# Optimization experiments

Hardware: AMD Instinct MI355X
Metric: run time of the kernel (lower is better)

Reference implementation:

```python
import jax, jax.numpy as jnp
import numpy as np

B, S, IN = 4, 4096, 2048
E, D, A, R = 16, 128, 128, 4  # num_experts, expert_vector_dim, attn_dim, mlp_rank
LN_EPS = 1e-5


def _ln2(x, g, b):
    # LayerNorm over the last two dims [E, D] jointly (torch nn.LayerNorm([E, D]))
    mu = x.mean(axis=(-2, -1), keepdims=True)
    var = ((x - mu) ** 2).mean(axis=(-2, -1), keepdims=True)
    return (x - mu) * jax.lax.rsqrt(var + LN_EPS) * g + b


def setup_inputs() -> dict:
    key = jax.random.key(0)
    ks = jax.random.split(key, 8)
    f32 = jnp.float32
    return {
        "hidden_states": jax.random.normal(ks[0], (B, S, IN), f32),
        "expert_embedding": jax.random.normal(ks[1], (E, D), f32) * 0.02,
        "ln_gamma": jnp.ones((E, D), f32),
        "ln_beta": jnp.zeros((E, D), f32),
        "Wv_w": jax.random.normal(ks[2], (E, IN), f32) * 0.02,
        "Wv_b": jnp.zeros((E,), f32),
        "mlp_w1": jax.random.normal(ks[3], (R, IN), f32) * 0.02,
        "mlp_b1": jnp.zeros((R,), f32),
        "mlp_w2": jax.random.normal(ks[4], (E * D, R), f32) * 0.02,
        "mlp_b2": jnp.zeros((E * D,), f32),
        "te_Wq": jax.random.normal(ks[5], (A, D), f32) * 0.05,
        "te_Wk": jax.random.normal(ks[6], (A, D), f32) * 0.05,
        "top_k": 2,
    }


def reference(hidden_states, expert_embedding, ln_gamma, ln_beta, Wv_w, Wv_b,
              mlp_w1, mlp_b1, mlp_w2, mlp_b2, te_Wq, te_Wk, top_k):
    # global expert vectors, layernormed over [E, D]: (E, D)
    ge = _ln2(expert_embedding[None, None], ln_gamma, ln_beta)[0, 0]
    # input gate = W_v(hidden): (B, S, E)
    input_gate = jnp.einsum('bsi,ei->bse', hidden_states, Wv_w) + Wv_b
    # TE mlp -> dynamic per-token expert vectors: (B, S, E, D)
    h = jax.nn.relu(jnp.einsum('bsi,ri->bsr', hidden_states, mlp_w1) + mlp_b1)
    dyn = (jnp.einsum('bsr,or->bso', h, mlp_w2) + mlp_b2).reshape(B, S, E, D)
    dyn = _ln2(dyn, ln_gamma, ln_beta)
    # attention-style routing: Q from dyn experts, K from global experts
    q = jnp.einsum('bsed,ad->bsea', dyn, te_Wq)     # (B, S, E, A)
    k = jnp.einsum('ed,ad->ea', ge, te_Wk)          # (E, A)
    scale = 1.0 / float(np.sqrt(A))
    sim = jax.nn.softmax(jnp.einsum('bsqa,ka->bsqk', q, k) * scale, axis=-1)
    gate = jnp.einsum('bsqk,bsk->bsq', sim, input_gate)
    rw = jax.nn.softmax(gate, axis=-1)              # (B, S, E)
    # top-k masking + sharpened softmax (temperature 0.1)
    vals, idx = jax.lax.top_k(rw, top_k)            # (B, S, k)
    oh = jax.nn.one_hot(idx, E, dtype=rw.dtype)     # (B, S, k, E)
    scattered = jnp.einsum('bske,bsk->bse', oh, vals)
    keep = oh.sum(axis=-2) > 0
    neg = jnp.finfo(rw.dtype).min
    masked = jnp.where(keep, scattered, neg)
    return jax.nn.softmax(masked / 0.1, axis=-1)
```

## Files before the change

kernel.cpp:

```cpp
#include <hip/hip_runtime.h>
#include <math.h>

#define NTOK   16384
#define INDIM  2048
#define NEXP   16
#define DDIM   128
#define NROWS  20

#define WS_PKT  0
#define WS_D1K  1024
#define WS_GQK  1280
#define WS_BQK  1536
#define WS_SCAL 1792
#define WS_TOT  1818

#define SIM_SCALE 0.08838834764831845f

__global__ __launch_bounds__(256) void hr_pre2(
    const float* __restrict__ ee, const float* __restrict__ gam,
    const float* __restrict__ bta, const float* __restrict__ w2,
    const float* __restrict__ b2, const float* __restrict__ wq,
    const float* __restrict__ wk, float* __restrict__ ws)
{
    const int tid  = threadIdx.x;
    const int bx   = blockIdx.x;
    const int lane = tid & 63;
    const int wave = tid >> 6;

    if (bx == 16) {
        __shared__ float sacc[26];
        if (tid < 26) sacc[tid] = 0.f;
        __syncthreads();
        float pa[26];
        #pragma unroll
        for (int j = 0; j < 26; ++j) pa[j] = 0.f;
        for (int i = tid; i < 2048; i += 256) {
            float b = b2[i];
            float4 w4 = *(const float4*)(w2 + i * 4);
            float wr[4] = {w4.x, w4.y, w4.z, w4.w};
            pa[0] += b;
            pa[1] += b * b;
            #pragma unroll
            for (int r = 0; r < 4; ++r) {
                pa[2 + r] += wr[r];
                pa[6 + r] += b * wr[r];
                #pragma unroll
                for (int r2 = 0; r2 < 4; ++r2) pa[10 + r * 4 + r2] += wr[r] * wr[r2];
            }
        }
        #pragma unroll
        for (int j = 0; j < 26; ++j) {
            float v = pa[j];
            v += __shfl_xor(v, 32);
            v += __shfl_xor(v, 16);
            v += __shfl_xor(v, 8);
            v += __shfl_xor(v, 4);
            v += __shfl_xor(v, 2);
            v += __shfl_xor(v, 1);
            if (lane == 0) atomicAdd(&sacc[j], v);
        }
        __syncthreads();
        if (tid < 26) ws[WS_SCAL + tid] = sacc[tid] * (1.f / 2048.f);
        return;
    }

    const int e2 = bx;
    __shared__ float sge[128];
    __shared__ float sK[128];
    __shared__ float sWqK[128];
    __shared__ float sred[8];

    float v8[8];
    float s = 0.f;
    #pragma unroll
    for (int j = 0; j < 8; ++j) {
        v8[j] = ee[tid + j * 256];
        s += v8[j];
    }
    s += __shfl_xor(s, 32); s += __shfl_xor(s, 16); s += __shfl_xor(s, 8);
    s += __shfl_xor(s, 4);  s += __shfl_xor(s, 2);  s += __shfl_xor(s, 1);
    if (lane == 0) sred[wave] = s;
    __syncthreads();
    const float mu = (sred[0] + sred[1] + sred[2] + sred[3]) * (1.f / 2048.f);
    float q = 0.f;
    #pragma unroll
    for (int j = 0; j < 8; ++j) {
        float d = v8[j] - mu;
        q += d * d;
    }
    q += __shfl_xor(q, 32); q += __shfl_xor(q, 16); q += __shfl_xor(q, 8);
    q += __shfl_xor(q, 4);  q += __shfl_xor(q, 2);  q += __shfl_xor(q, 1);
    if (lane == 0) sred[4 + wave] = q;
    __syncthreads();
    const float rsq = rsqrtf((sred[4] + sred[5] + sred[6] + sred[7]) * (1.f / 2048.f) + 1e-5f);

    if (tid < 128) {
        int idx = (e2 << 7) + tid;
        sge[tid] = (ee[idx] - mu) * rsq * gam[idx] + bta[idx];
    }
    __syncthreads();

    {
        int a = tid >> 1, half = tid & 1;
        const float* wr = wk + (a << 7) + (half << 6);
        const float* gg = sge + (half << 6);
        float acc = 0.f;
        #pragma unroll 8
        for (int j = 0; j < 64; ++j) acc = fmaf(gg[j], wr[j], acc);
        acc += __shfl_xor(acc, 1);
        if (half == 0) sK[a] = acc;
    }
    __syncthreads();

    {
        int d = tid >> 1, half = tid & 1;
        float acc = 0.f;
        #pragma unroll 8
        for (int j = 0; j < 64; ++j) {
            int a = (half << 6) + j;
            acc = fmaf(wq[(a << 7) + d], sK[a], acc);
        }
        acc += __shfl_xor(acc, 1);
        if (half == 0) sWqK[d] = acc;
    }
    __syncthreads();

    {
        int o = tid >> 2, qd = tid & 3;
        int r = o >> 4, e = o & 15;
        float acc = 0.f;
        #pragma unroll 8
        for (int j = 0; j < 32; ++j) {
            int d  = (qd << 5) + j;
            int ed = (e << 7) + d;
            acc = fmaf(w2[ed * 4 + r] * gam[ed], sWqK[d], acc);
        }
        acc += __shfl_xor(acc, 1);
        acc += __shfl_xor(acc, 2);
        if (qd == 0) ws[WS_PKT + (e2 << 6) + (r << 4) + e] = acc;
    }

    if (tid < 192) {
        int kind = tid >> 6;
        int e    = (tid >> 2) & 15;
        int qd   = tid & 3;
        float acc = 0.f;
        #pragma unroll 8
        for (int j = 0; j < 32; ++j) {
            int d  = (qd << 5) + j;
            int ed = (e << 7) + d;
            float w = sWqK[d];
            float t = (kind == 0) ? b2[ed] * gam[ed]
                    : (kind == 1) ? gam[ed]
                                  : bta[ed];
            acc = fmaf(t, w, acc);
        }
        acc += __shfl_xor(acc, 1);
        acc += __shfl_xor(acc, 2);
        if (qd == 0) ws[WS_D1K + (kind << 8) + (e2 << 4) + e] = acc;
    }
}

__global__ __launch_bounds__(256) void hr_main(
    const float* __restrict__ hidden, const float* __restrict__ wv,
    const float* __restrict__ wvb, const float* __restrict__ w1,
    const float* __restrict__ b1, const float* __restrict__ tab,
    float* __restrict__ out)
{
    __shared__ float tabs[1824];
    __shared__ float red[16][20];
    const int tid  = threadIdx.x;
    const int wave = tid >> 6;
    const int lane = tid & 63;

    for (int i = tid; i < WS_TOT; i += 256) tabs[i] = tab[i];

    const int tok0 = (blockIdx.x << 4) + (wave << 2);
    const float* hb = hidden + (size_t)tok0 * INDIM + (lane << 2);

    float acc[NROWS][4];
    #pragma unroll
    for (int w = 0; w < NROWS; ++w) {
        acc[w][0] = 0.f; acc[w][1] = 0.f; acc[w][2] = 0.f; acc[w][3] = 0.f;
    }

    for (int c = 0; c < 8; ++c) {
        const int off = c << 8;
        float4 h0 = *(const float4*)(hb + off);
        float4 h1 = *(const float4*)(hb + off + INDIM);
        float4 h2 = *(const float4*)(hb + off + 2 * INDIM);
        float4 h3 = *(const float4*)(hb + off + 3 * INDIM);
        #pragma unroll
        for (int w = 0; w < NROWS; ++w) {
            const float* wr = (w < 16) ? (wv + (w << 11)) : (w1 + ((w - 16) << 11));
            float4 wf = *(const float4*)(wr + off + (lane << 2));
            acc[w][0] = fmaf(h0.x, wf.x, fmaf(h0.y, wf.y, fmaf(h0.z, wf.z, fmaf(h0.w, wf.w, acc[w][0]))));
            acc[w][1] = fmaf(h1.x, wf.x, fmaf(h1.y, wf.y, fmaf(h1.z, wf.z, fmaf(h1.w, wf.w, acc[w][1]))));
            acc[w][2] = fmaf(h2.x, wf.x, fmaf(h2.y, wf.y, fmaf(h2.z, wf.z, fmaf(h2.w, wf.w, acc[w][2]))));
            acc[w][3] = fmaf(h3.x, wf.x, fmaf(h3.y, wf.y, fmaf(h3.z, wf.z, fmaf(h3.w, wf.w, acc[w][3]))));
        }
    }

    #pragma unroll
    for (int w = 0; w < NROWS; ++w) {
        #pragma unroll
        for (int t = 0; t < 4; ++t) {
            float v = acc[w][t];
            v += __shfl_xor(v, 32);
            v += __shfl_xor(v, 16);
            v += __shfl_xor(v, 8);
            v += __shfl_xor(v, 4);
            v += __shfl_xor(v, 2);
            v += __shfl_xor(v, 1);
            acc[w][t] = v;
        }
    }
    if (lane < 4) {
        const int row = (wave << 2) + lane;
        #pragma unroll
        for (int w = 0; w < NROWS; ++w) {
            float v = (lane == 0) ? acc[w][0]
                    : (lane == 1) ? acc[w][1]
                    : (lane == 2) ? acc[w][2] : acc[w][3];
            red[row][w] = v;
        }
    }
    __syncthreads();

    const int tok = tid >> 4;
    const int e   = tid & 15;

    float ig[16];
    #pragma unroll
    for (int j = 0; j < 16; ++j) ig[j] = red[tok][j] + wvb[j];
    float h[4];
    #pragma unroll
    for (int r = 0; r < 4; ++r) h[r] = fmaxf(red[tok][16 + r] + b1[r], 0.f);

    float muT = tabs[WS_SCAL + 0];
    float e2m = tabs[WS_SCAL + 1];
    #pragma unroll
    for (int r = 0; r < 4; ++r) {
        muT = fmaf(h[r], tabs[WS_SCAL + 2 + r], muT);
        e2m = fmaf(2.f * h[r], tabs[WS_SCAL + 6 + r], e2m);
        #pragma unroll
        for (int r2 = 0; r2 < 4; ++r2)
            e2m = fmaf(h[r] * h[r2], tabs[WS_SCAL + 10 + r * 4 + r2], e2m);
    }
    const float var = e2m - muT * muT;
    const float rsq = rsqrtf(var + 1e-5f);

    float sv[16];
    #pragma unroll
    for (int e2 = 0; e2 < 16; ++e2) {
        float s = tabs[WS_D1K + (e2 << 4) + e];
        s = fmaf(h[0], tabs[(e2 << 6) + e], s);
        s = fmaf(h[1], tabs[(e2 << 6) + 16 + e], s);
        s = fmaf(h[2], tabs[(e2 << 6) + 32 + e], s);
        s = fmaf(h[3], tabs[(e2 << 6) + 48 + e], s);
        s = fmaf(-muT, tabs[WS_GQK + (e2 << 4) + e], s);
        sv[e2] = (rsq * s + tabs[WS_BQK + (e2 << 4) + e]) * SIM_SCALE;
    }
    float mx = sv[0];
    #pragma unroll
    for (int e2 = 1; e2 < 16; ++e2) mx = fmaxf(mx, sv[e2]);
    float den = 0.f, gate = 0.f;
    #pragma unroll
    for (int e2 = 0; e2 < 16; ++e2) {
        float p = __expf(sv[e2] - mx);
        den += p;
        gate = fmaf(p, ig[e2], gate);
    }
    gate /= den;

    float gm = gate;
    gm = fmaxf(gm, __shfl_xor(gm, 1));
    gm = fmaxf(gm, __shfl_xor(gm, 2));
    gm = fmaxf(gm, __shfl_xor(gm, 4));
    gm = fmaxf(gm, __shfl_xor(gm, 8));
    float ex = __expf(gate - gm);
    float es = ex;
    es += __shfl_xor(es, 1);
    es += __shfl_xor(es, 2);
    es += __shfl_xor(es, 4);
    es += __shfl_xor(es, 8);
    const float rw = ex / es;

    float v1 = rw; int i1 = e;
    #pragma unroll
    for (int m = 1; m <= 8; m <<= 1) {
        float ov = __shfl_xor(v1, m);
        int   oi = __shfl_xor(i1, m);
        if (ov > v1 || (ov == v1 && oi < i1)) { v1 = ov; i1 = oi; }
    }
    float v2 = (e == i1) ? -INFINITY : rw; int i2 = e;
    #pragma unroll
    for (int m = 1; m <= 8; m <<= 1) {
        float ov = __shfl_xor(v2, m);
        int   oi = __shfl_xor(i2, m);
        if (ov > v2 || (ov == v2 && oi < i2)) { v2 = ov; i2 = oi; }
    }

    float oval = 0.f;
    if (e == i1 || e == i2) {
        float t = __expf((v2 - v1) * 10.f);
        oval = (e == i1) ? (1.f / (1.f + t)) : (t / (1.f + t));
    }
    out[(((size_t)blockIdx.x << 4) + tok) * 16 + e] = oval;
}

extern "C" void kernel_launch(void* const* d_in, const int* in_sizes, int n_in,
                              void* d_out, int out_size, void* d_ws, size_t ws_size,
                              hipStream_t stream)
{
    const float* hidden = (const float*)d_in[0];
    const float* ee     = (const float*)d_in[1];
    const float* gam    = (const float*)d_in[2];
    const float* bta    = (const float*)d_in[3];
    const float* wv     = (const float*)d_in[4];
    const float* wvb    = (const float*)d_in[5];
    const float* w1     = (const float*)d_in[6];
    const float* b1     = (const float*)d_in[7];
    const float* w2     = (const float*)d_in[8];
    const float* b2     = (const float*)d_in[9];
    const float* wq     = (const float*)d_in[10];
    const float* wk     = (const float*)d_in[11];
    float* out = (float*)d_out;
    float* ws  = (float*)d_ws;

    hipLaunchKernelGGL(hr_pre2, dim3(17), dim3(256), 0, stream,
                       ee, gam, bta, w2, b2, wq, wk, ws);
    hipLaunchKernelGGL(hr_main, dim3(NTOK / 16), dim3(256), 0, stream,
                       hidden, wv, wvb, w1, b1, ws, out);
}
```

Measured before the change: 267.7 us.

## Double-buffer weight rows into LDS via async global_load_lds and restructure reduction

The main GEMV loop now stages the 20 weight rows per 256-column chunk into LDS with asynchronous global-to-LDS loads, double-buffered so the next chunk's weights and hidden values load while the current chunk computes. The cross-lane reduction is cut to two shuffles, with the rest finished through a padded LDS transpose and summed per (token,row). The routing table is read straight from global memory instead of being copied into shared memory. Launch bounds request 3 blocks per CU. This trades redundant per-wave global weight loads and long shuffle chains for more LDS traffic and extra barriers.

```diff
diff --git a/kernel.cpp b/kernel.cpp
--- a/kernel.cpp
+++ b/kernel.cpp
@@ -3,9 +3,9 @@
 
 #define NTOK   16384
 #define INDIM  2048
-#define NEXP   16
-#define DDIM   128
 #define NROWS  20
+#define CHUNK  256
+#define NCH    8
 
 #define WS_PKT  0
 #define WS_D1K  1024
@@ -15,6 +15,53 @@
 #define WS_TOT  1818
 
 #define SIM_SCALE 0.08838834764831845f
+
+#define LBUF1   5120
+#define LRED2_STRIDE 324
+#define LRED    5440
+
+__device__ __forceinline__ void async16(const float* g, float* l) {
+    __builtin_amdgcn_global_load_lds(
+        (const __attribute__((address_space(1))) void*)g,
+        (__attribute__((address_space(3))) void*)l, 16, 0, 0);
+}
+
+__device__ __forceinline__ void stage_rows(const float* __restrict__ wv,
+                                           const float* __restrict__ w1,
+                                           float* ldsbase, int wave, int lane,
+                                           int goff) {
+    const int l4 = lane << 2;
+    #pragma unroll
+    for (int j = 0; j < 5; ++j) {
+        const int r = wave + (j << 2);
+        const float* src = (j < 4) ? (wv + (r << 11)) : (w1 + ((r - 16) << 11));
+        async16(src + goff + l4, ldsbase + r * CHUNK + l4);
+    }
+}
+
+__device__ __forceinline__ void load_h(float4* hr, const float* hb, int c) {
+    const float* p = hb + (c << 8);
+    hr[0] = *(const float4*)(p);
+    hr[1] = *(const float4*)(p + INDIM);
+    hr[2] = *(const float4*)(p + 2 * INDIM);
+    hr[3] = *(const float4*)(p + 3 * INDIM);
+}
+
+__device__ __forceinline__ void compute_chunk(float acc[NROWS][4],
+                                              const float* wb,
+                                              const float4 h[4]) {
+    #pragma unroll
+    for (int w = 0; w < NROWS; ++w) {
+        float4 wf = *(const float4*)(wb + (w << 8));
+        #pragma unroll
+        for (int t = 0; t < 4; ++t) {
+            acc[w][t] = fmaf(h[t].x, wf.x,
+                        fmaf(h[t].y, wf.y,
+                        fmaf(h[t].z, wf.z,
+                        fmaf(h[t].w, wf.w, acc[w][t]))));
+        }
+    }
+}
 
 __global__ __launch_bounds__(256) void hr_pre2(
     const float* __restrict__ ee, const float* __restrict__ gam,
@@ -51,12 +98,8 @@
         #pragma unroll
         for (int j = 0; j < 26; ++j) {
             float v = pa[j];
-            v += __shfl_xor(v, 32);
-            v += __shfl_xor(v, 16);
-            v += __shfl_xor(v, 8);
-            v += __shfl_xor(v, 4);
-            v += __shfl_xor(v, 2);
-            v += __shfl_xor(v, 1);
+            v += __shfl_xor(v, 32); v += __shfl_xor(v, 16); v += __shfl_xor(v, 8);
+            v += __shfl_xor(v, 4);  v += __shfl_xor(v, 2);  v += __shfl_xor(v, 1);
             if (lane == 0) atomicAdd(&sacc[j], v);
         }
         __syncthreads();
@@ -73,10 +116,7 @@
     float v8[8];
     float s = 0.f;
     #pragma unroll
-    for (int j = 0; j < 8; ++j) {
-        v8[j] = ee[tid + j * 256];
-        s += v8[j];
-    }
+    for (int j = 0; j < 8; ++j) { v8[j] = ee[tid + j * 256]; s += v8[j]; }
     s += __shfl_xor(s, 32); s += __shfl_xor(s, 16); s += __shfl_xor(s, 8);
     s += __shfl_xor(s, 4);  s += __shfl_xor(s, 2);  s += __shfl_xor(s, 1);
     if (lane == 0) sred[wave] = s;
@@ -84,10 +124,7 @@
     const float mu = (sred[0] + sred[1] + sred[2] + sred[3]) * (1.f / 2048.f);
     float q = 0.f;
     #pragma unroll
-    for (int j = 0; j < 8; ++j) {
-        float d = v8[j] - mu;
-        q += d * d;
-    }
+    for (int j = 0; j < 8; ++j) { float d = v8[j] - mu; q += d * d; }
     q += __shfl_xor(q, 32); q += __shfl_xor(q, 16); q += __shfl_xor(q, 8);
     q += __shfl_xor(q, 4);  q += __shfl_xor(q, 2);  q += __shfl_xor(q, 1);
     if (lane == 0) sred[4 + wave] = q;
@@ -161,20 +198,17 @@
     }
 }
 
-__global__ __launch_bounds__(256) void hr_main(
+__global__ __launch_bounds__(256, 3) void hr_main(
     const float* __restrict__ hidden, const float* __restrict__ wv,
     const float* __restrict__ wvb, const float* __restrict__ w1,
     const float* __restrict__ b1, const float* __restrict__ tab,
     float* __restrict__ out)
 {
-    __shared__ float tabs[1824];
-    __shared__ float red[16][20];
+    __shared__ float lds[10240];
+
     const int tid  = threadIdx.x;
     const int wave = tid >> 6;
     const int lane = tid & 63;
-
-    for (int i = tid; i < WS_TOT; i += 256) tabs[i] = tab[i];
-
     const int tok0 = (blockIdx.x << 4) + (wave << 2);
     const float* hb = hidden + (size_t)tok0 * INDIM + (lane << 2);
 
@@ -184,21 +218,23 @@
         acc[w][0] = 0.f; acc[w][1] = 0.f; acc[w][2] = 0.f; acc[w][3] = 0.f;
     }
 
-    for (int c = 0; c < 8; ++c) {
-        const int off = c << 8;
-        float4 h0 = *(const float4*)(hb + off);
-        float4 h1 = *(const float4*)(hb + off + INDIM);
-        float4 h2 = *(const float4*)(hb + off + 2 * INDIM);
-        float4 h3 = *(const float4*)(hb + off + 3 * INDIM);
-        #pragma unroll
-        for (int w = 0; w < NROWS; ++w) {
-            const float* wr = (w < 16) ? (wv + (w << 11)) : (w1 + ((w - 16) << 11));
-            float4 wf = *(const float4*)(wr + off + (lane << 2));
-            acc[w][0] = fmaf(h0.x, wf.x, fmaf(h0.y, wf.y, fmaf(h0.z, wf.z, fmaf(h0.w, wf.w, acc[w][0]))));
-            acc[w][1] = fmaf(h1.x, wf.x, fmaf(h1.y, wf.y, fmaf(h1.z, wf.z, fmaf(h1.w, wf.w, acc[w][1]))));
-            acc[w][2] = fmaf(h2.x, wf.x, fmaf(h2.y, wf.y, fmaf(h2.z, wf.z, fmaf(h2.w, wf.w, acc[w][2]))));
-            acc[w][3] = fmaf(h3.x, wf.x, fmaf(h3.y, wf.y, fmaf(h3.z, wf.z, fmaf(h3.w, wf.w, acc[w][3]))));
-        }
+    float4 ha[4], hob[4];
+    stage_rows(wv, w1, lds, wave, lane, 0);
+    load_h(ha, hb, 0);
+    __syncthreads();
+
+    for (int cc = 0; cc < 4; ++cc) {
+        const int c1 = 2 * cc + 1;
+        stage_rows(wv, w1, lds + LBUF1, wave, lane, c1 << 8);
+        load_h(hob, hb, c1);
+        compute_chunk(acc, &lds[lane << 2], ha);
+        __syncthreads();
+        if (cc != 3) {
+            stage_rows(wv, w1, lds, wave, lane, (c1 + 1) << 8);
+            load_h(ha, hb, c1 + 1);
+        }
+        compute_chunk(acc, &lds[LBUF1 + (lane << 2)], hob);
+        __syncthreads();
     }
 
     #pragma unroll
@@ -208,21 +244,32 @@
             float v = acc[w][t];
             v += __shfl_xor(v, 32);
             v += __shfl_xor(v, 16);
-            v += __shfl_xor(v, 8);
-            v += __shfl_xor(v, 4);
-            v += __shfl_xor(v, 2);
-            v += __shfl_xor(v, 1);
             acc[w][t] = v;
         }
     }
-    if (lane < 4) {
-        const int row = (wave << 2) + lane;
+    {
+        const int q = lane >> 4, i = lane & 15;
         #pragma unroll
         for (int w = 0; w < NROWS; ++w) {
-            float v = (lane == 0) ? acc[w][0]
-                    : (lane == 1) ? acc[w][1]
-                    : (lane == 2) ? acc[w][2] : acc[w][3];
-            red[row][w] = v;
+            if (q == w / 5) {
+                #pragma unroll
+                for (int t = 0; t < 4; ++t)
+                    lds[((wave << 2) + t) * LRED2_STRIDE + (w << 4) + i] = acc[w][t];
+            }
+        }
+    }
+    __syncthreads();
+
+    #pragma unroll
+    for (int pp = 0; pp < 2; ++pp) {
+        const int p = tid + pp * 256;
+        if (p < 320) {
+            const int w = p >> 4, tok = p & 15;
+            const float4* rp = (const float4*)&lds[tok * LRED2_STRIDE + (w << 4)];
+            float4 r0 = rp[0], r1 = rp[1], r2 = rp[2], r3 = rp[3];
+            float s = (r0.x + r0.y + r0.z + r0.w) + (r1.x + r1.y + r1.z + r1.w)
+                    + (r2.x + r2.y + r2.z + r2.w) + (r3.x + r3.y + r3.z + r3.w);
+            lds[LRED + tok * 20 + w] = s;
         }
     }
     __syncthreads();
@@ -232,20 +279,20 @@
 
     float ig[16];
     #pragma unroll
-    for (int j = 0; j < 16; ++j) ig[j] = red[tok][j] + wvb[j];
+    for (int j = 0; j < 16; ++j) ig[j] = lds[LRED + tok * 20 + j] + wvb[j];
     float h[4];
     #pragma unroll
-    for (int r = 0; r < 4; ++r) h[r] = fmaxf(red[tok][16 + r] + b1[r], 0.f);
-
-    float muT = tabs[WS_SCAL + 0];
-    float e2m = tabs[WS_SCAL + 1];
+    for (int r = 0; r < 4; ++r) h[r] = fmaxf(lds[LRED + tok * 20 + 16 + r] + b1[r], 0.f);
+
+    float muT = tab[WS_SCAL + 0];
+    float e2m = tab[WS_SCAL + 1];
     #pragma unroll
     for (int r = 0; r < 4; ++r) {
-        muT = fmaf(h[r], tabs[WS_SCAL + 2 + r], muT);
-        e2m = fmaf(2.f * h[r], tabs[WS_SCAL + 6 + r], e2m);
+        muT = fmaf(h[r], tab[WS_SCAL + 2 + r], muT);
+        e2m = fmaf(2.f * h[r], tab[WS_SCAL + 6 + r], e2m);
         #pragma unroll
         for (int r2 = 0; r2 < 4; ++r2)
-            e2m = fmaf(h[r] * h[r2], tabs[WS_SCAL + 10 + r * 4 + r2], e2m);
+            e2m = fmaf(h[r] * h[r2], tab[WS_SCAL + 10 + r * 4 + r2], e2m);
     }
     const float var = e2m - muT * muT;
     const float rsq = rsqrtf(var + 1e-5f);
@@ -253,13 +300,13 @@
     float sv[16];
     #pragma unroll
     for (int e2 = 0; e2 < 16; ++e2) {
-        float s = tabs[WS_D1K + (e2 << 4) + e];
-        s = fmaf(h[0], tabs[(e2 << 6) + e], s);
-        s = fmaf(h[1], tabs[(e2 << 6) + 16 + e], s);
-        s = fmaf(h[2], tabs[(e2 << 6) + 32 + e], s);
-        s = fmaf(h[3], tabs[(e2 << 6) + 48 + e], s);
-        s = fmaf(-muT, tabs[WS_GQK + (e2 << 4) + e], s);
-        sv[e2] = (rsq * s + tabs[WS_BQK + (e2 << 4) + e]) * SIM_SCALE;
+        float s = tab[WS_D1K + (e2 << 4) + e];
+        s = fmaf(h[0], tab[(e2 << 6) + e], s);
+        s = fmaf(h[1], tab[(e2 << 6) + 16 + e], s);
+        s = fmaf(h[2], tab[(e2 << 6) + 32 + e], s);
+        s = fmaf(h[3], tab[(e2 << 6) + 48 + e], s);
+        s = fmaf(-muT, tab[WS_GQK + (e2 << 4) + e], s);
+        sv[e2] = (rsq * s + tab[WS_BQK + (e2 << 4) + e]) * SIM_SCALE;
     }
     float mx = sv[0];
     #pragma unroll
```

After: 336.0 us. +25.5%, slower.
